# Performance work log

Measured on AMD Instinct MI355X. Metric: run time of the kernel, lower is better.

## Reference

```python
import jax, jax.numpy as jnp
import numpy as np

# ---- ATSSPostProcessor config ----
PRE_NMS_THRESH = 0.05
PRE_NMS_TOP_N  = 400      # k candidates per image (pre_nms_top_n)
NMS_THRESH     = 0.4
POST_TOP_N     = 100      # fpn_post_nms_top_n
MIN_SIZE       = 0.0
NUM_ANGLE_BINS = 90
BBOX_W         = (10.0, 10.0, 5.0, 5.0)   # box_coder xywh weights; angle is passthrough (argmax-90 deg)
N, C, H, W     = 4, 15, 256, 256           # A=1 anchor per location
STRIDE, ANCHOR_SIZE = 8.0, 64.0
MAXV = 16                                   # vertex buffer for quad-quad clipping


def setup_inputs():
    key = jax.random.key(0)
    k1, k2, k3, k4 = jax.random.split(key, 4)
    box_cls = jax.random.normal(k1, (N, C, H, W), jnp.float32) - 2.0  # sigmoid ~0.12 avg -> plenty of candidates
    box_regression = jax.random.normal(k2, (N, 4, H, W), jnp.float32) * 0.5
    centerness = jax.random.normal(k3, (N, 1, H, W), jnp.float32)
    angle = jax.random.normal(k4, (N, NUM_ANGLE_BINS, H, W), jnp.float32)
    # xywha anchors on the stride-8 grid, row-major (H, W) to match permute_and_flatten ordering
    ys, xs = jnp.meshgrid(jnp.arange(H, dtype=jnp.float32), jnp.arange(W, dtype=jnp.float32), indexing='ij')
    cx = (xs.reshape(-1) + 0.5) * STRIDE
    cy = (ys.reshape(-1) + 0.5) * STRIDE
    wh = jnp.full((H * W,), ANCHOR_SIZE, jnp.float32)
    a0 = jnp.zeros((H * W,), jnp.float32)
    anchors = jnp.broadcast_to(jnp.stack([cx, cy, wh, wh, a0], -1), (N, H * W, 5))
    return {"box_cls": box_cls, "box_regression": box_regression, "centerness": centerness,
            "angle": angle, "anchors": jnp.asarray(anchors)}


def xywha_to_corners(b):
    # b [..., 5] (cx,cy,w,h,angle_deg) -> [..., 4, 2], CCW order
    cx, cy, w, h, a = b[..., 0], b[..., 1], b[..., 2], b[..., 3], b[..., 4]
    t = a * (jnp.pi / 180.0)
    c, s = jnp.cos(t), jnp.sin(t)
    ox = jnp.asarray([1., -1., -1., 1.], b.dtype) * (w[..., None] * 0.5)
    oy = jnp.asarray([1., 1., -1., -1.], b.dtype) * (h[..., None] * 0.5)
    x = cx[..., None] + ox * c[..., None] - oy * s[..., None]
    y = cy[..., None] + ox * s[..., None] + oy * c[..., None]
    return jnp.stack([x, y], -1)


def _clip_edge(poly, n, p1, p2):
    # Sutherland-Hodgman: clip CCW polygon (poly[:n]) against half-plane left of p1->p2
    e = p2 - p1
    d = e[0] * (poly[:, 1] - p1[1]) - e[1] * (poly[:, 0] - p1[0])  # >= 0 is inside
    def body(i, carry):
        out, m = carry
        j = jnp.where(i == n - 1, 0, i + 1)
        cur, nxt, dc, dn = poly[i], poly[j], d[i], d[j]
        denom = dc - dn
        denom = jnp.where(jnp.abs(denom) < 1e-8, 1e-8, denom)
        ip = cur + (dc / denom) * (nxt - cur)
        act = i < n
        a1 = act & (dc >= 0)
        out = out.at[m].set(jnp.where(a1, cur, out[m]))
        m = m + a1.astype(jnp.int32)
        a2 = act & ((dc >= 0) != (dn >= 0))
        out = out.at[m].set(jnp.where(a2, ip, out[m]))
        m = m + a2.astype(jnp.int32)
        return out, m
    return jax.lax.fori_loop(0, 8, body, (jnp.zeros_like(poly), jnp.int32(0)))


def _quad_inter_area(c1, c2):
    # intersection area of two CCW quads via polygon clipping + shoelace
    poly = jnp.zeros((MAXV, 2), c1.dtype).at[:4].set(c1)
    n = jnp.int32(4)
    def edge(e, carry):
        poly, n = carry
        return _clip_edge(poly, n, c2[e], c2[(e + 1) % 4])
    poly, n = jax.lax.fori_loop(0, 4, edge, (poly, n))
    idx = jnp.arange(MAXV)
    j = jnp.where(idx == n - 1, 0, idx + 1)
    mask = idx < n
    terms = poly[:, 0] * poly[j, 1] - poly[j, 0] * poly[:, 1]
    return 0.5 * jnp.abs(jnp.sum(jnp.where(mask, terms, 0.0)))


def _riou_matrix(boxes):                        # [k,5] -> [k,k] rotated IoU
    corners = xywha_to_corners(boxes)           # [k,4,2]
    areas = boxes[:, 2] * boxes[:, 3]
    def one(ci, ai):
        def two(cj, aj):
            inter = _quad_inter_area(ci, cj)
            return inter / (ai + aj - inter + 1e-7)
        return jax.vmap(two)(corners, areas)
    return jax.vmap(one)(corners, areas)


@jax.jit
def _forward(box_cls, box_regression, centerness, angle, anchors):
    n, c, h, w = box_cls.shape
    K, k = h * w, PRE_NMS_TOP_N
    # permute_and_flatten + activations
    cls = jax.nn.sigmoid(box_cls).transpose(0, 2, 3, 1).reshape(n, K, c)
    reg = box_regression.transpose(0, 2, 3, 1).reshape(n, K, 4)
    ctr = jax.nn.sigmoid(centerness).reshape(n, K)
    ang = jax.nn.softmax(angle.transpose(0, 2, 3, 1).reshape(n, K, NUM_ANGLE_BINS), axis=-1)
    # pre-nms threshold on raw sigmoid cls, topk on cls*centerness
    cand = cls > PRE_NMS_THRESH
    comb = cls * ctr[:, :, None]
    flat = jnp.where(cand, comb, -1.0).reshape(n, K * c)
    topv, topi = jax.lax.top_k(flat, k)          # sorted descending
    valid = topv > 0.0                           # emulates per_pre_nms_top_n clamp
    loc = topi // c
    labels = topi % c + 1
    reg_s = jnp.take_along_axis(reg, loc[..., None], axis=1)       # [n,k,4]
    anc_s = jnp.take_along_axis(anchors, loc[..., None], axis=1)   # [n,k,5]
    ang_s = jnp.take_along_axis(ang, loc[..., None], axis=1)       # [n,k,90]
    pred_angle = jnp.argmax(ang_s, axis=-1).astype(reg_s.dtype) - 90.0
    # box_coder.decode (xywh deltas, angle passthrough)
    wx, wy, ww, wh = BBOX_W
    dx, dy = reg_s[..., 0] / wx, reg_s[..., 1] / wy
    dw = jnp.clip(reg_s[..., 2] / ww, -10.0, 4.0)
    dh = jnp.clip(reg_s[..., 3] / wh, -10.0, 4.0)
    acx, acy, aw, ah = anc_s[..., 0], anc_s[..., 1], anc_s[..., 2], anc_s[..., 3]
    boxes = jnp.stack([dx * aw + acx, dy * ah + acy,
                       aw * jnp.exp(dw), ah * jnp.exp(dh), pred_angle], -1)
    valid = valid & (boxes[..., 2] >= MIN_SIZE) & (boxes[..., 3] >= MIN_SIZE)
    scores = jnp.where(valid, jnp.sqrt(jnp.maximum(topv, 0.0)), 0.0)
    # class-aware rotated NMS (boxlist_ml_rnms): IoU only within same class
    iou = jax.lax.stop_gradient(jax.vmap(_riou_matrix)(boxes))     # [n,k,k]
    same = labels[:, :, None] == labels[:, None, :]
    iou = jnp.where(same, iou, 0.0)
    idxs = jnp.arange(k)
    def body(i, keep):
        sup = keep[:, i][:, None] & (iou[:, i, :] > NMS_THRESH) & (idxs[None, :] > i)
        return keep & ~sup
    keep = jax.lax.fori_loop(0, k, body, valid)
    # keep top fpn_post_nms_top_n by score
    fscore = jnp.where(keep, scores, -1.0)
    fv, fi = jax.lax.top_k(fscore, POST_TOP_N)
    fvalid = fv > 0.0
    fboxes = jnp.take_along_axis(boxes, fi[..., None], axis=1)
    flabels = jnp.take_along_axis(labels, fi, axis=1)
    corners = xywha_to_corners(fboxes).reshape(n, POST_TOP_N, 8)   # convert('xyxyxyxy')
    out = jnp.concatenate([corners,
                           jnp.maximum(fv, 0.0)[..., None],
                           flabels.astype(corners.dtype)[..., None],
                           fvalid.astype(corners.dtype)[..., None]], -1)
    return out * fvalid[..., None].astype(out.dtype)   # [N, POST_TOP_N, 11]


def reference(box_cls, box_regression, centerness, angle, anchors):
    return _forward(box_cls, box_regression, centerness, angle, anchors)
```

## Files before the change

### kernel.cpp

```cpp
#include <hip/hip_runtime.h>
#include <math.h>

#define NIMG 4
#define NCLS 15
#define HDIM 256
#define WDIM 256
#define HW (HDIM*WDIM)
#define NANG 90
#define KTOP 400
#define POSTN 100
#define NBINS 4096
#define CAP 4096
#define PAIRCAP 81920

#define HIST_OFF   0
#define CNT_OFF    65536
#define TBIN_OFF   65600
#define PCNT_OFF   65664
#define SUPT_OFF   65728
#define ZERO_BYTES 166080
#define CAND_OFF   166080
#define SKEY_OFF   297152
#define COR_OFF    309952
#define AREA_OFF   361152
#define LAB_OFF    367552
#define SC_OFF     373952
#define VAL_OFF    380352
#define CCX_OFF    386752
#define CCY_OFF    393152
#define CRAD_OFF   399552
#define PAIRS_OFF  405952

__device__ __forceinline__ float sigmoidf(float x) {
    return 1.0f / (1.0f + expf(-x));
}

__global__ void k_hist(const float* __restrict__ cls, const float* __restrict__ ctr,
                       int* __restrict__ hist) {
    __shared__ int sh[NBINS];
    const int n = blockIdx.y;
    const int p = blockIdx.x * 256 + threadIdx.x;
    for (int b = threadIdx.x; b < NBINS; b += 256) sh[b] = 0;
    __syncthreads();
    float cv = sigmoidf(ctr[n * HW + p]);
    for (int j = 0; j < NCLS; ++j) {
        float s = sigmoidf(cls[(n * NCLS + j) * HW + p]);
        if (s > 0.05f) {
            float comb = s * cv;
            int b = (int)(comb * 4096.0f);
            b = b < 0 ? 0 : (b > NBINS - 1 ? NBINS - 1 : b);
            atomicAdd(&sh[b], 1);
        }
    }
    __syncthreads();
    for (int b = threadIdx.x; b < NBINS; b += 256) {
        int v = sh[b];
        if (v) atomicAdd(&hist[n * NBINS + b], v);
    }
}

__global__ void k_thresh(const int* __restrict__ hist, int* __restrict__ tbin) {
    const int n = blockIdx.x;
    __shared__ int sh[NBINS];
    __shared__ int part[256];
    for (int b = threadIdx.x; b < NBINS; b += 256) sh[b] = hist[n * NBINS + b];
    __syncthreads();
    int s = 0;
    int base = threadIdx.x * 16;
    for (int b = 0; b < 16; ++b) s += sh[base + b];
    part[threadIdx.x] = s;
    __syncthreads();
    if (threadIdx.x == 0) {
        int acc = 0, seg = -1, above = 0;
        for (int sg = 255; sg >= 0; --sg) {
            int ps = part[sg];
            if (acc + ps >= KTOP) { seg = sg; above = acc; break; }
            acc += ps;
        }
        int t = 0;
        if (seg >= 0) {
            int a2 = above;
            t = seg * 16;
            for (int b = seg * 16 + 15; b >= seg * 16; --b) {
                a2 += sh[b];
                if (a2 >= KTOP) { t = b; break; }
            }
        }
        tbin[n] = t;
    }
}

__global__ void k_collect(const float* __restrict__ cls, const float* __restrict__ ctr,
                          const int* __restrict__ tbin, int* __restrict__ cnt,
                          unsigned long long* __restrict__ cand) {
    const int n = blockIdx.y;
    const int p = blockIdx.x * 256 + threadIdx.x;
    const int t = tbin[n];
    float cv = sigmoidf(ctr[n * HW + p]);
    for (int j = 0; j < NCLS; ++j) {
        float s = sigmoidf(cls[(n * NCLS + j) * HW + p]);
        if (s > 0.05f) {
            float comb = s * cv;
            int b = (int)(comb * 4096.0f);
            b = b < 0 ? 0 : (b > NBINS - 1 ? NBINS - 1 : b);
            if (b >= t) {
                int pos = atomicAdd(&cnt[n], 1);
                if (pos < CAP) {
                    unsigned int fb = __float_as_uint(comb);
                    unsigned int idx = (unsigned int)(p * NCLS + j);
                    cand[n * CAP + pos] =
                        ((unsigned long long)fb << 32) | (unsigned long long)(~idx);
                }
            }
        }
    }
}

__global__ __launch_bounds__(256)
void k_select(const unsigned long long* __restrict__ cand, const int* __restrict__ cnt,
              unsigned long long* __restrict__ skey) {
    const int n = blockIdx.x;
    __shared__ unsigned long long key[CAP];
    int c = cnt[n];
    if (c > CAP) c = CAP;
    int S = 512;
    while (S < c) S <<= 1;
    for (int t = threadIdx.x; t < S; t += 256)
        key[t] = (t < c) ? cand[n * CAP + t] : 0ULL;
    __syncthreads();
    for (int k = 2; k <= S; k <<= 1) {
        for (int j = k >> 1; j > 0; j >>= 1) {
            for (int i = threadIdx.x; i < S; i += 256) {
                int l = i ^ j;
                if (l > i) {
                    unsigned long long a = key[i], b = key[l];
                    bool up = ((i & k) == 0);
                    if ((a > b) == up) { key[i] = b; key[l] = a; }
                }
            }
            __syncthreads();
        }
    }
    for (int r = threadIdx.x; r < KTOP; r += 256)
        skey[n * KTOP + r] = key[S - 1 - r];
}

__global__ __launch_bounds__(64)
void k_decode(const unsigned long long* __restrict__ skey,
              const float* __restrict__ reg, const float* __restrict__ ang,
              const float* __restrict__ anchors,
              float* __restrict__ cor, float* __restrict__ area, int* __restrict__ lab,
              float* __restrict__ sc, int* __restrict__ val,
              float* __restrict__ ccx, float* __restrict__ ccy, float* __restrict__ crad) {
#pragma clang fp contract(off)
    const int r = blockIdx.x;
    const int n = blockIdx.y;
    const int l = threadIdx.x;
    const int base = n * KTOP + r;
    unsigned long long kk = skey[base];
    if (kk == 0ULL) {
        if (l == 0) {
            val[base] = 0; sc[base] = 0.0f; lab[base] = 0; area[base] = 0.0f;
            ccx[base] = 0.0f; ccy[base] = 0.0f; crad[base] = 0.0f;
            for (int q = 0; q < 8; ++q) cor[base * 8 + q] = 0.0f;
        }
        return;
    }
    unsigned int idx = ~((unsigned int)kk);
    int loc = (int)(idx / 15u);
    const float* ap = ang + ((size_t)n * NANG) * HW + loc;
    float bv = -INFINITY; int bb = 1000;
    for (int b = l; b < NANG; b += 64) {
        float v = ap[(size_t)b * HW];
        if (v > bv) { bv = v; bb = b; }
    }
    for (int off = 32; off > 0; off >>= 1) {
        float ov = __shfl_down(bv, off);
        int   ob = __shfl_down(bb, off);
        if (ov > bv || (ov == bv && ob < bb)) { bv = ov; bb = ob; }
    }
    if (l == 0) {
        int cl = (int)(idx % 15u);
        float topv = __uint_as_float((unsigned int)(kk >> 32));
        const float* rp = reg + ((size_t)n * 4) * HW + loc;
        float dx = rp[0] / 10.0f;
        float dy = rp[HW] / 10.0f;
        float dw = rp[2 * (size_t)HW] / 5.0f;
        float dh = rp[3 * (size_t)HW] / 5.0f;
        dw = fminf(fmaxf(dw, -10.0f), 4.0f);
        dh = fminf(fmaxf(dh, -10.0f), 4.0f);
        const float* an = anchors + ((size_t)n * HW + loc) * 5;
        float acx = an[0], acy = an[1], aw = an[2], ah = an[3];
        float bcx = dx * aw + acx;
        float bcy = dy * ah + acy;
        float bw = aw * expf(dw);
        float bh = ah * expf(dh);
        float pa = (float)bb - 90.0f;
        float th = pa * (float)0.017453292519943295;
        float cth = cosf(th), sth = sinf(th);
        float hw2 = bw * 0.5f, hh2 = bh * 0.5f;
        const float oxs[4] = {1.0f, -1.0f, -1.0f, 1.0f};
        const float oys[4] = {1.0f, 1.0f, -1.0f, -1.0f};
        for (int q = 0; q < 4; ++q) {
            float ox = oxs[q] * hw2, oy = oys[q] * hh2;
            cor[base * 8 + 2 * q]     = bcx + ox * cth - oy * sth;
            cor[base * 8 + 2 * q + 1] = bcy + ox * sth + oy * cth;
        }
        val[base] = 1;
        sc[base] = sqrtf(topv);
        lab[base] = cl + 1;
        area[base] = bw * bh;
        ccx[base] = bcx; ccy[base] = bcy;
        crad[base] = 0.5f * sqrtf(bw * bw + bh * bh);
    }
}

__device__ __forceinline__ float arr_get8(const float* a, int idx) {
    float r = a[0];
#pragma unroll
    for (int s = 1; s < 8; ++s) r = (s == idx) ? a[s] : r;
    return r;
}
__device__ __forceinline__ void arr_set8(float* a, int idx, float v) {
#pragma unroll
    for (int s = 0; s < 8; ++s) a[s] = (s == idx) ? v : a[s];
}

__device__ float quad_inter_area(const float* c1x, const float* c1y,
                                 const float* c2x, const float* c2y) {
#pragma clang fp contract(off)
    float px[8], py[8], qx[8], qy[8];
    int n = 4;
#pragma unroll
    for (int i = 0; i < 8; ++i) { px[i] = (i < 4) ? c1x[i] : 0.0f;
                                  py[i] = (i < 4) ? c1y[i] : 0.0f;
                                  qx[i] = 0.0f; qy[i] = 0.0f; }
#pragma unroll
    for (int e = 0; e < 4; ++e) {
        float p1x = c2x[e], p1y = c2y[e];
        int e2 = (e + 1) & 3;
        float ex = c2x[e2] - p1x, ey = c2y[e2] - p1y;
        int m = 0;
#pragma unroll
        for (int i = 0; i < 8; ++i) {
            if (i < n) {
                int j = (i == n - 1) ? 0 : i + 1;
                float cxi = px[i], cyi = py[i];
                float cxj = arr_get8(px, j), cyj = arr_get8(py, j);
                float dc = ex * (cyi - p1y) - ey * (cxi - p1x);
                float dn = ex * (cyj - p1y) - ey * (cxj - p1x);
                bool ic = (dc >= 0.0f), in2 = (dn >= 0.0f);
                if (ic) { arr_set8(qx, m, cxi); arr_set8(qy, m, cyi); ++m; }
                if (ic != in2) {
                    float denom = dc - dn;
                    if (fabsf(denom) < 1e-8f) denom = 1e-8f;
                    float tp = dc / denom;
                    arr_set8(qx, m, cxi + tp * (cxj - cxi));
                    arr_set8(qy, m, cyi + tp * (cyj - cyi));
                    ++m;
                }
            }
        }
        n = m;
        if (n == 0) return 0.0f;
#pragma unroll
        for (int i = 0; i < 8; ++i) { px[i] = qx[i]; py[i] = qy[i]; }
    }
    float ssum = 0.0f;
#pragma unroll
    for (int i = 0; i < 8; ++i) {
        if (i < n) {
            int j = (i == n - 1) ? 0 : i + 1;
            ssum += px[i] * arr_get8(py, j) - arr_get8(px, j) * py[i];
        }
    }
    return 0.5f * fabsf(ssum);
}

__global__ __launch_bounds__(256)
void k_prefilter(const int* __restrict__ lab,
                 const float* __restrict__ ccx, const float* __restrict__ ccy,
                 const float* __restrict__ crad,
                 int* __restrict__ pcnt, int* __restrict__ pairs) {
    const int n = blockIdx.y;
    const int p = blockIdx.x * 256 + threadIdx.x;
    if (p >= KTOP * KTOP) return;
    const int i = p / KTOP;
    const int j = p - i * KTOP;
    if (j <= i) return;
    const int base = n * KTOP;
    const int li = lab[base + i];
    if (li == 0 || lab[base + j] != li) return;
    float dx = ccx[base + i] - ccx[base + j];
    float dy = ccy[base + i] - ccy[base + j];
    float rr = crad[base + i] + crad[base + j];
    if (dx * dx + dy * dy > rr * rr) return;
    int pos = atomicAdd(&pcnt[n], 1);
    if (pos < PAIRCAP) pairs[n * PAIRCAP + pos] = (i << 16) | j;
}

__global__ __launch_bounds__(256)
void k_iou(const int* __restrict__ pcnt, const int* __restrict__ pairs,
           const float* __restrict__ cor, const float* __restrict__ area,
           unsigned long long* __restrict__ supT) {
#pragma clang fp contract(off)
    const int n = blockIdx.y;
    int c = pcnt[n];
    if (c > PAIRCAP) c = PAIRCAP;
    const int t = blockIdx.x * 256 + threadIdx.x;
    if (t >= c) return;
    const int pr = pairs[n * PAIRCAP + t];
    const int i = pr >> 16;
    const int j = pr & 0xffff;
    const int base = n * KTOP;
    float cix[4], ciy[4], cjx[4], cjy[4];
    for (int q = 0; q < 4; ++q) {
        cix[q] = cor[(base + i) * 8 + 2 * q]; ciy[q] = cor[(base + i) * 8 + 2 * q + 1];
        cjx[q] = cor[(base + j) * 8 + 2 * q]; cjy[q] = cor[(base + j) * 8 + 2 * q + 1];
    }
    float inter = quad_inter_area(cix, ciy, cjx, cjy);
    float iou = inter / (area[base + i] + area[base + j] - inter + 1e-7f);
    if (iou > 0.4f) {
        atomicOr(&supT[((size_t)(n * 7 + (j >> 6)) * 7 + (i >> 6)) * 64 + (j & 63)],
                 1ULL << (i & 63));
    }
}

__global__ __launch_bounds__(64)
void k_nms_out(const unsigned long long* __restrict__ supT,
               const int* __restrict__ val,
               const float* __restrict__ cor, const float* __restrict__ sc,
               const int* __restrict__ lab, float* __restrict__ out) {
    const int n = blockIdx.x;
    const int l = threadIdx.x;
    unsigned removed = 0;
#pragma unroll
    for (int t = 0; t < 7; ++t) {
        int r = 64 * t + l;
        int v = (r < KTOP) ? val[n * KTOP + r] : 0;
        if (!v) removed |= (1u << t);
    }
    unsigned long long cm[7][7];
#pragma unroll
    for (int t = 0; t < 7; ++t)
#pragma unroll
        for (int rb = 0; rb < 7; ++rb)
            cm[t][rb] = supT[((size_t)(n * 7 + t) * 7 + rb) * 64 + l];
#pragma unroll
    for (int rb = 0; rb < 7; ++rb) {
        const int lim = (rb == 6) ? (KTOP - 384) : 64;
        for (int ib = 0; ib < lim; ++ib) {
            unsigned rm = (unsigned)__builtin_amdgcn_readlane((int)removed, ib);
            if (!((rm >> rb) & 1u)) {
                removed |= ((unsigned)((cm[0][rb] >> ib) & 1ULL));
                removed |= ((unsigned)((cm[1][rb] >> ib) & 1ULL)) << 1;
                removed |= ((unsigned)((cm[2][rb] >> ib) & 1ULL)) << 2;
                removed |= ((unsigned)((cm[3][rb] >> ib) & 1ULL)) << 3;
                removed |= ((unsigned)((cm[4][rb] >> ib) & 1ULL)) << 4;
                removed |= ((unsigned)((cm[5][rb] >> ib) & 1ULL)) << 5;
                removed |= ((unsigned)((cm[6][rb] >> ib) & 1ULL)) << 6;
            }
        }
    }
    __shared__ int order[POSTN];
    int rank = 0;
#pragma unroll
    for (int t = 0; t < 7; ++t) {
        bool kb = !((removed >> t) & 1u) && (64 * t + l < KTOP);
        unsigned long long m = __ballot(kb);
        int my = rank + __popcll(m & ((1ULL << l) - 1ULL));
        if (kb && my < POSTN) order[my] = 64 * t + l;
        rank += __popcll(m);
    }
    int kcnt = rank < POSTN ? rank : POSTN;
    __syncthreads();
    for (int e = l; e < POSTN * 11; e += 64) {
        int r = e / 11, c = e - r * 11;
        float v = 0.0f;
        if (r < kcnt) {
            int i = order[r];
            int b = n * KTOP + i;
            if (c < 8)       v = cor[b * 8 + c];
            else if (c == 8) v = sc[b];
            else if (c == 9) v = (float)lab[b];
            else             v = 1.0f;
        }
        out[(n * POSTN + r) * 11 + c] = v;
    }
}

extern "C" void kernel_launch(void* const* d_in, const int* in_sizes, int n_in,
                              void* d_out, int out_size, void* d_ws, size_t ws_size,
                              hipStream_t stream) {
    const float* box_cls = (const float*)d_in[0];
    const float* box_reg = (const float*)d_in[1];
    const float* ctr     = (const float*)d_in[2];
    const float* ang     = (const float*)d_in[3];
    const float* anchors = (const float*)d_in[4];
    float* out = (float*)d_out;
    char* ws = (char*)d_ws;

    int* hist = (int*)(ws + HIST_OFF);
    int* cnt  = (int*)(ws + CNT_OFF);
    int* tbin = (int*)(ws + TBIN_OFF);
    int* pcnt = (int*)(ws + PCNT_OFF);
    unsigned long long* supT = (unsigned long long*)(ws + SUPT_OFF);
    unsigned long long* cand = (unsigned long long*)(ws + CAND_OFF);
    unsigned long long* skey = (unsigned long long*)(ws + SKEY_OFF);
    float* cor  = (float*)(ws + COR_OFF);
    float* area = (float*)(ws + AREA_OFF);
    int* lab    = (int*)(ws + LAB_OFF);
    float* sc   = (float*)(ws + SC_OFF);
    int* val    = (int*)(ws + VAL_OFF);
    float* ccx  = (float*)(ws + CCX_OFF);
    float* ccy  = (float*)(ws + CCY_OFF);
    float* crad = (float*)(ws + CRAD_OFF);
    int* pairs  = (int*)(ws + PAIRS_OFF);

    hipMemsetAsync(d_ws, 0, ZERO_BYTES, stream);
    k_hist     <<<dim3(HW / 256, NIMG), 256, 0, stream>>>(box_cls, ctr, hist);
    k_thresh   <<<NIMG, 256, 0, stream>>>(hist, tbin);
    k_collect  <<<dim3(HW / 256, NIMG), 256, 0, stream>>>(box_cls, ctr, tbin, cnt, cand);
    k_select   <<<NIMG, 256, 0, stream>>>(cand, cnt, skey);
    k_decode   <<<dim3(KTOP, NIMG), 64, 0, stream>>>(skey, box_reg, ang, anchors,
                                                     cor, area, lab, sc, val, ccx, ccy, crad);
    k_prefilter<<<dim3((KTOP * KTOP + 255) / 256, NIMG), 256, 0, stream>>>(
                   lab, ccx, ccy, crad, pcnt, pairs);
    k_iou      <<<dim3(PAIRCAP / 256, NIMG), 256, 0, stream>>>(pcnt, pairs, cor, area, supT);
    k_nms_out  <<<NIMG, 64, 0, stream>>>(supT, val, cor, sc, lab, out);
}
```

Baseline: 268.4 us.

## Fuse threshold into collect, merge prefilter with IoU, vectorize score loads

Folds the top-k threshold search into each collect block, so every block recomputes it from the global histogram. The pair prefilter and rotated IoU become one kernel, which drops the pair list and its atomic compaction. Histogram and collect now read four pixels per thread with float4 loads. Together this removes two launches and the pair buffer round trip, at the cost of redundant threshold work per block and divergent IoU work inside warps.

New measurement: 256.9 us. 1.04x faster.

```diff
diff --git a/kernel.cpp b/kernel.cpp
--- a/kernel.cpp
+++ b/kernel.cpp
@@ -3,53 +3,54 @@
 
 #define NIMG 4
 #define NCLS 15
-#define HDIM 256
-#define WDIM 256
-#define HW (HDIM*WDIM)
+#define HW 65536
 #define NANG 90
 #define KTOP 400
 #define POSTN 100
 #define NBINS 4096
 #define CAP 4096
-#define PAIRCAP 81920
 
 #define HIST_OFF   0
 #define CNT_OFF    65536
-#define TBIN_OFF   65600
-#define PCNT_OFF   65664
-#define SUPT_OFF   65728
-#define ZERO_BYTES 166080
-#define CAND_OFF   166080
-#define SKEY_OFF   297152
-#define COR_OFF    309952
-#define AREA_OFF   361152
-#define LAB_OFF    367552
-#define SC_OFF     373952
-#define VAL_OFF    380352
-#define CCX_OFF    386752
-#define CCY_OFF    393152
-#define CRAD_OFF   399552
-#define PAIRS_OFF  405952
+#define SUPT_OFF   65600
+#define ZERO_BYTES 165952
+#define CAND_OFF   165952
+#define SKEY_OFF   297024
+#define COR_OFF    309824
+#define AREA_OFF   361024
+#define LAB_OFF    367424
+#define SC_OFF     373824
+#define VAL_OFF    380224
+#define CCX_OFF    386624
+#define CCY_OFF    393024
+#define CRAD_OFF   399424
 
 __device__ __forceinline__ float sigmoidf(float x) {
     return 1.0f / (1.0f + expf(-x));
 }
 
-__global__ void k_hist(const float* __restrict__ cls, const float* __restrict__ ctr,
-                       int* __restrict__ hist) {
+__global__ __launch_bounds__(256)
+void k_hist(const float* __restrict__ cls, const float* __restrict__ ctr,
+            int* __restrict__ hist) {
     __shared__ int sh[NBINS];
     const int n = blockIdx.y;
-    const int p = blockIdx.x * 256 + threadIdx.x;
+    const int p4 = (blockIdx.x * 256 + threadIdx.x) * 4;
     for (int b = threadIdx.x; b < NBINS; b += 256) sh[b] = 0;
     __syncthreads();
-    float cv = sigmoidf(ctr[n * HW + p]);
+    float4 cv4 = *(const float4*)(ctr + n * HW + p4);
+    float cv[4] = {sigmoidf(cv4.x), sigmoidf(cv4.y), sigmoidf(cv4.z), sigmoidf(cv4.w)};
     for (int j = 0; j < NCLS; ++j) {
-        float s = sigmoidf(cls[(n * NCLS + j) * HW + p]);
-        if (s > 0.05f) {
-            float comb = s * cv;
-            int b = (int)(comb * 4096.0f);
-            b = b < 0 ? 0 : (b > NBINS - 1 ? NBINS - 1 : b);
-            atomicAdd(&sh[b], 1);
+        float4 s4 = *(const float4*)(cls + (size_t)(n * NCLS + j) * HW + p4);
+        float sv[4] = {s4.x, s4.y, s4.z, s4.w};
+#pragma unroll
+        for (int e = 0; e < 4; ++e) {
+            float s = sigmoidf(sv[e]);
+            if (s > 0.05f) {
+                float comb = s * cv[e];
+                int b = (int)(comb * 4096.0f);
+                b = b < 0 ? 0 : (b > NBINS - 1 ? NBINS - 1 : b);
+                atomicAdd(&sh[b], 1);
+            }
         }
     }
     __syncthreads();
@@ -59,57 +60,62 @@
     }
 }
 
-__global__ void k_thresh(const int* __restrict__ hist, int* __restrict__ tbin) {
-    const int n = blockIdx.x;
-    __shared__ int sh[NBINS];
+__global__ __launch_bounds__(256)
+void k_collect(const float* __restrict__ cls, const float* __restrict__ ctr,
+               const int* __restrict__ hist, int* __restrict__ cnt,
+               unsigned long long* __restrict__ cand) {
+    const int n = blockIdx.y;
     __shared__ int part[256];
-    for (int b = threadIdx.x; b < NBINS; b += 256) sh[b] = hist[n * NBINS + b];
-    __syncthreads();
-    int s = 0;
-    int base = threadIdx.x * 16;
-    for (int b = 0; b < 16; ++b) s += sh[base + b];
-    part[threadIdx.x] = s;
-    __syncthreads();
-    if (threadIdx.x == 0) {
-        int acc = 0, seg = -1, above = 0;
-        for (int sg = 255; sg >= 0; --sg) {
-            int ps = part[sg];
-            if (acc + ps >= KTOP) { seg = sg; above = acc; break; }
-            acc += ps;
-        }
-        int t = 0;
-        if (seg >= 0) {
-            int a2 = above;
-            t = seg * 16;
-            for (int b = seg * 16 + 15; b >= seg * 16; --b) {
-                a2 += sh[b];
-                if (a2 >= KTOP) { t = b; break; }
-            }
-        }
-        tbin[n] = t;
-    }
-}
-
-__global__ void k_collect(const float* __restrict__ cls, const float* __restrict__ ctr,
-                          const int* __restrict__ tbin, int* __restrict__ cnt,
-                          unsigned long long* __restrict__ cand) {
-    const int n = blockIdx.y;
-    const int p = blockIdx.x * 256 + threadIdx.x;
-    const int t = tbin[n];
-    float cv = sigmoidf(ctr[n * HW + p]);
+    __shared__ int s_t;
+    {
+        const int* hb = hist + n * NBINS;
+        int s = 0;
+        int base = threadIdx.x * 16;
+        for (int b = 0; b < 16; ++b) s += hb[base + b];
+        part[threadIdx.x] = s;
+        __syncthreads();
+        if (threadIdx.x == 0) {
+            int acc = 0, seg = -1, above = 0;
+            for (int sg = 255; sg >= 0; --sg) {
+                int ps = part[sg];
+                if (acc + ps >= KTOP) { seg = sg; above = acc; break; }
+                acc += ps;
+            }
+            int t = 0;
+            if (seg >= 0) {
+                int a2 = above;
+                t = seg * 16;
+                for (int b = seg * 16 + 15; b >= seg * 16; --b) {
+                    a2 += hb[b];
+                    if (a2 >= KTOP) { t = b; break; }
+                }
+            }
+            s_t = t;
+        }
+        __syncthreads();
+    }
+    const int t = s_t;
+    const int p4 = (blockIdx.x * 256 + threadIdx.x) * 4;
+    float4 cv4 = *(const float4*)(ctr + n * HW + p4);
+    float cv[4] = {sigmoidf(cv4.x), sigmoidf(cv4.y), sigmoidf(cv4.z), sigmoidf(cv4.w)};
     for (int j = 0; j < NCLS; ++j) {
-        float s = sigmoidf(cls[(n * NCLS + j) * HW + p]);
-        if (s > 0.05f) {
-            float comb = s * cv;
-            int b = (int)(comb * 4096.0f);
-            b = b < 0 ? 0 : (b > NBINS - 1 ? NBINS - 1 : b);
-            if (b >= t) {
-                int pos = atomicAdd(&cnt[n], 1);
-                if (pos < CAP) {
-                    unsigned int fb = __float_as_uint(comb);
-                    unsigned int idx = (unsigned int)(p * NCLS + j);
-                    cand[n * CAP + pos] =
-                        ((unsigned long long)fb << 32) | (unsigned long long)(~idx);
+        float4 s4 = *(const float4*)(cls + (size_t)(n * NCLS + j) * HW + p4);
+        float sv[4] = {s4.x, s4.y, s4.z, s4.w};
+#pragma unroll
+        for (int e = 0; e < 4; ++e) {
+            float s = sigmoidf(sv[e]);
+            if (s > 0.05f) {
+                float comb = s * cv[e];
+                int b = (int)(comb * 4096.0f);
+                b = b < 0 ? 0 : (b > NBINS - 1 ? NBINS - 1 : b);
+                if (b >= t) {
+                    int pos = atomicAdd(&cnt[n], 1);
+                    if (pos < CAP) {
+                        unsigned int fb  = __float_as_uint(comb);
+                        unsigned int idx = (unsigned int)((p4 + e) * NCLS + j);
+                        cand[n * CAP + pos] =
+                            ((unsigned long long)fb << 32) | (unsigned long long)(~idx);
+                    }
                 }
             }
         }
@@ -278,10 +284,12 @@
 }
 
 __global__ __launch_bounds__(256)
-void k_prefilter(const int* __restrict__ lab,
-                 const float* __restrict__ ccx, const float* __restrict__ ccy,
-                 const float* __restrict__ crad,
-                 int* __restrict__ pcnt, int* __restrict__ pairs) {
+void k_pairs(const float* __restrict__ cor, const float* __restrict__ area,
+             const int* __restrict__ lab,
+             const float* __restrict__ ccx, const float* __restrict__ ccy,
+             const float* __restrict__ crad,
+             unsigned long long* __restrict__ supT) {
+#pragma clang fp contract(off)
     const int n = blockIdx.y;
     const int p = blockIdx.x * 256 + threadIdx.x;
     if (p >= KTOP * KTOP) return;
@@ -295,24 +303,6 @@
     float dy = ccy[base + i] - ccy[base + j];
     float rr = crad[base + i] + crad[base + j];
     if (dx * dx + dy * dy > rr * rr) return;
-    int pos = atomicAdd(&pcnt[n], 1);
-    if (pos < PAIRCAP) pairs[n * PAIRCAP + pos] = (i << 16) | j;
-}
-
-__global__ __launch_bounds__(256)
-void k_iou(const int* __restrict__ pcnt, const int* __restrict__ pairs,
-           const float* __restrict__ cor, const float* __restrict__ area,
-           unsigned long long* __restrict__ supT) {
-#pragma clang fp contract(off)
-    const int n = blockIdx.y;
-    int c = pcnt[n];
-    if (c > PAIRCAP) c = PAIRCAP;
-    const int t = blockIdx.x * 256 + threadIdx.x;
-    if (t >= c) return;
-    const int pr = pairs[n * PAIRCAP + t];
-    const int i = pr >> 16;
-    const int j = pr & 0xffff;
-    const int base = n * KTOP;
     float cix[4], ciy[4], cjx[4], cjy[4];
     for (int q = 0; q < 4; ++q) {
         cix[q] = cor[(base + i) * 8 + 2 * q]; ciy[q] = cor[(base + i) * 8 + 2 * q + 1];
@@ -402,8 +392,6 @@
 
     int* hist = (int*)(ws + HIST_OFF);
     int* cnt  = (int*)(ws + CNT_OFF);
-    int* tbin = (int*)(ws + TBIN_OFF);
-    int* pcnt = (int*)(ws + PCNT_OFF);
     unsigned long long* supT = (unsigned long long*)(ws + SUPT_OFF);
     unsigned long long* cand = (unsigned long long*)(ws + CAND_OFF);
     unsigned long long* skey = (unsigned long long*)(ws + SKEY_OFF);
@@ -415,17 +403,14 @@
     float* ccx  = (float*)(ws + CCX_OFF);
     float* ccy  = (float*)(ws + CCY_OFF);
     float* crad = (float*)(ws + CRAD_OFF);
-    int* pairs  = (int*)(ws + PAIRS_OFF);
 
     hipMemsetAsync(d_ws, 0, ZERO_BYTES, stream);
-    k_hist     <<<dim3(HW / 256, NIMG), 256, 0, stream>>>(box_cls, ctr, hist);
-    k_thresh   <<<NIMG, 256, 0, stream>>>(hist, tbin);
-    k_collect  <<<dim3(HW / 256, NIMG), 256, 0, stream>>>(box_cls, ctr, tbin, cnt, cand);
-    k_select   <<<NIMG, 256, 0, stream>>>(cand, cnt, skey);
-    k_decode   <<<dim3(KTOP, NIMG), 64, 0, stream>>>(skey, box_reg, ang, anchors,
-                                                     cor, area, lab, sc, val, ccx, ccy, crad);
-    k_prefilter<<<dim3((KTOP * KTOP + 255) / 256, NIMG), 256, 0, stream>>>(
-                   lab, ccx, ccy, crad, pcnt, pairs);
-    k_iou      <<<dim3(PAIRCAP / 256, NIMG), 256, 0, stream>>>(pcnt, pairs, cor, area, supT);
-    k_nms_out  <<<NIMG, 64, 0, stream>>>(supT, val, cor, sc, lab, out);
-}
+    k_hist   <<<dim3(HW / 1024, NIMG), 256, 0, stream>>>(box_cls, ctr, hist);
+    k_collect<<<dim3(HW / 1024, NIMG), 256, 0, stream>>>(box_cls, ctr, hist, cnt, cand);
+    k_select <<<NIMG, 256, 0, stream>>>(cand, cnt, skey);
+    k_decode <<<dim3(KTOP, NIMG), 64, 0, stream>>>(skey, box_reg, ang, anchors,
+                                                   cor, area, lab, sc, val, ccx, ccy, crad);
+    k_pairs  <<<dim3((KTOP * KTOP + 255) / 256, NIMG), 256, 0, stream>>>(
+                 cor, area, lab, ccx, ccy, crad, supT);
+    k_nms_out<<<NIMG, 64, 0, stream>>>(supT, val, cor, sc, lab, out);
+}
```
